# Kernel tuning notes

Measured on AMD Instinct MI355X. Metric: run time of the kernel, lower is better.

Reference implementation:

```python
import jax, jax.numpy as jnp
import numpy as np

PT, SKIP, CNN_UNITS, RNN_UNITS = 16, 32, 512, 512


def setup_inputs() -> dict:
    key = jax.random.key(0)
    k_x, k_w, k_u = jax.random.split(key, 3)
    B, T, C, H = 128, 512, CNN_UNITS, RNN_UNITS
    # 0.05 scaling keeps the relu GRU recurrence numerically stable
    x = jax.random.normal(k_x, (B, T, C), dtype=jnp.float32)
    W = jax.random.normal(k_w, (C, 3 * H), dtype=jnp.float32) * 0.05
    U = jax.random.normal(k_u, (H, 3 * H), dtype=jnp.float32) * 0.05
    b = jnp.zeros((2, 3 * H), dtype=jnp.float32)  # [input_bias, recurrent_bias] (reset_after=True)
    return {"x": x, "W": W, "U": U, "b": b}


def reference(x, W, U, b):
    B, T, C = x.shape
    H = U.shape[0]
    pt, skip = PT, SKIP
    # pretrans: last pt*skip steps -> (B, pt, skip, C) -> (B, skip, pt, C) -> (B*skip, pt, C)
    s = x[:, -pt * skip:, :]
    s = s.reshape(B, pt, skip, C).transpose(0, 2, 1, 3).reshape(B * skip, pt, C)
    # precompute input projections for all timesteps: (pt, B*skip, 3H)
    xp = jnp.einsum('ntc,ch->tnh', s, W) + b[0]
    b_rec = b[1]

    def step(h, xt):
        rec = h @ U + b_rec                      # (N, 3H)
        xz, xr, xh = jnp.split(xt, 3, axis=-1)
        rz, rr, rh = jnp.split(rec, 3, axis=-1)
        z = jax.nn.sigmoid(xz + rz)
        r = jax.nn.sigmoid(xr + rr)
        hh = jax.nn.relu(xh + r * rh)            # activation='relu'
        h_new = z * h + (1.0 - z) * hh
        return h_new, None

    h0 = jnp.zeros((B * skip, H), dtype=x.dtype)
    h_final, _ = jax.lax.scan(step, h0, xp)
    # posttrans: (B*skip, H) -> (B, skip*H)
    return h_final.reshape(B, skip * H)
```

## Files before the change

kernel.cpp:

```cpp
#include <hip/hip_runtime.h>
#include <cstddef>


typedef unsigned short u16;
typedef __attribute__((ext_vector_type(8))) short short8;
typedef __attribute__((ext_vector_type(8))) u16 u16x8;
typedef __attribute__((ext_vector_type(4))) float floatx4;

#define MFMA16(a, b, c) __builtin_amdgcn_mfma_f32_16x16x32_bf16((a), (b), (c), 0, 0, 0)

__device__ __forceinline__ u16 f32_to_bf16(float f) {
  union { float f; unsigned int u; } c; c.f = f;
  unsigned int u = c.u + 0x7FFFu + ((c.u >> 16) & 1u);
  return (u16)(u >> 16);
}
__device__ __forceinline__ float bf16_to_f32(u16 v) {
  union { unsigned int u; float f; } c; c.u = ((unsigned int)v) << 16;
  return c.f;
}
__device__ __forceinline__ float sigmoidf_(float x) {
  return 1.0f / (1.0f + __expf(-x));
}
__device__ __forceinline__ void gload_lds16(const void* g, void* l) {
  __builtin_amdgcn_global_load_lds(
      (const __attribute__((address_space(1))) unsigned int*)g,
      (__attribute__((address_space(3))) unsigned int*)l, 16, 0, 0);
}

__global__ __launch_bounds__(256)
void pack_x(const float* __restrict__ x, u16* __restrict__ xb) {
  __shared__ u16 sm[64 * 512];
  const int t = blockIdx.x >> 6;
  const int nb = blockIdx.x & 63;
  const int tid = threadIdx.x;
#pragma unroll
  for (int it = 0; it < 16; ++it) {
    int idx = it * 256 + tid;
    int row = idx >> 6, ch = idx & 63;
    int xrow = (nb * 2 + (row >> 5)) * 512 + t * 32 + (row & 31);
    const float* src = x + (size_t)xrow * 512 + ch * 8;
    floatx4 va = *(const floatx4*)src;
    floatx4 vb = *(const floatx4*)(src + 4);
    u16x8 pk;
    pk[0] = f32_to_bf16(va[0]); pk[1] = f32_to_bf16(va[1]);
    pk[2] = f32_to_bf16(va[2]); pk[3] = f32_to_bf16(va[3]);
    pk[4] = f32_to_bf16(vb[0]); pk[5] = f32_to_bf16(vb[1]);
    pk[6] = f32_to_bf16(vb[2]); pk[7] = f32_to_bf16(vb[3]);
    *(u16x8*)&sm[row * 512 + (ch ^ (row & 7)) * 8] = pk;
  }
  __syncthreads();
  u16* dst = xb + (size_t)blockIdx.x * 32768;
#pragma unroll
  for (int it = 0; it < 16; ++it) {
    int idx = it * 256 + tid;
    int row = idx & 63, g = (idx >> 6) & 3, kt = idx >> 8;
    int ch = kt * 4 + g;
    u16x8 vv = *(const u16x8*)&sm[row * 512 + (ch ^ (row & 7)) * 8];
    *(u16x8*)(dst + (size_t)idx * 8) = vv;
  }
}

__global__ void pack_Bt(const float* __restrict__ W, const float* __restrict__ U,
                        u16* __restrict__ Bt) {
  size_t gid = (size_t)blockIdx.x * 256 + threadIdx.x;
  int col = (int)(gid & 63);
  int g   = (int)((gid >> 6) & 3);
  int kt  = (int)((gid >> 8) & 31);
  int cc  = (int)(gid >> 13);
  int c = cc * 64 + col;
  int k0 = kt * 32 + g * 8;
  u16x8 pk;
#pragma unroll
  for (int j = 0; j < 8; ++j) {
    int k = k0 + j;
    float v = (k < 512) ? W[(size_t)k * 1536 + c] : U[(size_t)(k - 512) * 1536 + c];
    pk[j] = f32_to_bf16(v);
  }
  *(u16x8*)(Bt + gid * 8) = pk;
}

__global__ __launch_bounds__(256)
void gru_step(const u16* __restrict__ xb, const u16* __restrict__ Bt,
              const float* __restrict__ bias,
              const u16* __restrict__ h_in, u16* __restrict__ h_out,
              float* __restrict__ out, int t, int first, int last) {
  __shared__ alignas(16) char sm[32768];
  const int tid = threadIdx.x;
  const int idx = blockIdx.x;
  const int nb = ((idx >> 6) << 3) | (idx & 7);
  const int hb = (idx >> 3) & 7;
  const int w = __builtin_amdgcn_readfirstlane(tid >> 6);
  const int lane = tid & 63;
  const int wy = w >> 1, wx = w & 1;
  const int q = lane >> 4, lc = lane & 15;

  const u16* xbB = xb + (size_t)(t * 64 + nb) * 32768;
  const u16* htB = h_in + (size_t)nb * 32768;
  const int cs0 = hb, cs1 = 8 + hb, cs2 = 16 + hb;

  floatx4 acZ[2][2] = {{{0.f,0.f,0.f,0.f},{0.f,0.f,0.f,0.f}},{{0.f,0.f,0.f,0.f},{0.f,0.f,0.f,0.f}}};
  floatx4 acR[2][2] = {{{0.f,0.f,0.f,0.f},{0.f,0.f,0.f,0.f}},{{0.f,0.f,0.f,0.f},{0.f,0.f,0.f,0.f}}};
  floatx4 acX[2][2] = {{{0.f,0.f,0.f,0.f},{0.f,0.f,0.f,0.f}},{{0.f,0.f,0.f,0.f},{0.f,0.f,0.f,0.f}}};
  floatx4 acH[2][2] = {{{0.f,0.f,0.f,0.f},{0.f,0.f,0.f,0.f}},{{0.f,0.f,0.f,0.f},{0.f,0.f,0.f,0.f}}};

  const int ktall = first ? 16 : 32;
  const int wo = w * 1024;

  auto stage = [&](int kt, int bsel) {
    char* lds = sm + bsel * 16384;
    const char* aS = (const char*)((kt < 16) ? (xbB + (size_t)kt * 2048)
                                             : (htB + (size_t)(kt - 16) * 2048));
    gload_lds16(aS + wo + lane * 16, lds + wo);
    gload_lds16((const char*)(Bt + (size_t)(cs0 * 32 + kt) * 2048) + wo + lane * 16,
                lds + 4096 + wo);
    gload_lds16((const char*)(Bt + (size_t)(cs1 * 32 + kt) * 2048) + wo + lane * 16,
                lds + 8192 + wo);
    gload_lds16((const char*)(Bt + (size_t)(cs2 * 32 + kt) * 2048) + wo + lane * 16,
                lds + 12288 + wo);
  };

  auto compute = [&](int bsel, floatx4 (&acT)[2][2]) {
    const char* lds = sm + bsel * 16384;
    short8 a0 = *(const short8*)(lds + (q * 64 + wy * 32 + lc) * 16);
    short8 a1 = *(const short8*)(lds + (q * 64 + wy * 32 + 16 + lc) * 16);
#pragma unroll
    for (int ci = 0; ci < 2; ++ci) {
      int co = (q * 64 + wx * 32 + ci * 16 + lc) * 16;
      short8 bz = *(const short8*)(lds + 4096 + co);
      short8 br = *(const short8*)(lds + 8192 + co);
      short8 bh = *(const short8*)(lds + 12288 + co);
      acZ[0][ci] = MFMA16(a0, bz, acZ[0][ci]);
      acZ[1][ci] = MFMA16(a1, bz, acZ[1][ci]);
      acR[0][ci] = MFMA16(a0, br, acR[0][ci]);
      acR[1][ci] = MFMA16(a1, br, acR[1][ci]);
      acT[0][ci] = MFMA16(a0, bh, acT[0][ci]);
      acT[1][ci] = MFMA16(a1, bh, acT[1][ci]);
    }
  };

  stage(0, 0);
  __syncthreads();
  for (int kt = 0; kt < 16; ++kt) {
    if (kt + 1 < ktall) stage(kt + 1, (kt + 1) & 1);
    compute(kt & 1, acX);
    __syncthreads();
  }
  if (!first) {
    for (int kt = 16; kt < 32; ++kt) {
      if (kt + 1 < 32) stage(kt + 1, (kt + 1) & 1);
      compute(kt & 1, acH);
      __syncthreads();
    }
  }

  const float* b0 = bias;
  const float* b1 = bias + 1536;
  u16* Ct = (u16*)sm;
#pragma unroll
  for (int ci = 0; ci < 2; ++ci) {
    const int hcl = wx * 32 + ci * 16 + lc;
    const int hg = hb * 64 + hcl;
    const float bz = b0[hg] + b1[hg];
    const float br = b0[512 + hg] + b1[512 + hg];
    const float b0h = b0[1024 + hg];
    const float b1h = b1[1024 + hg];
    const int ktg = hg >> 5;
    const int gg = (hg >> 3) & 3;
    const size_t hbase = (((size_t)nb * 16 + ktg) * 4 + gg) * 64;
#pragma unroll
    for (int mi = 0; mi < 2; ++mi) {
#pragma unroll
      for (int reg = 0; reg < 4; ++reg) {
        const int nl = wy * 32 + mi * 16 + q * 4 + reg;
        const int n = nb * 64 + nl;
        float z = sigmoidf_(acZ[mi][ci][reg] + bz);
        float r = sigmoidf_(acR[mi][ci][reg] + br);
        float hh = acX[mi][ci][reg] + b0h + r * (acH[mi][ci][reg] + b1h);
        hh = fmaxf(hh, 0.0f);
        float hp = 0.0f;
        if (!first) hp = bf16_to_f32(h_in[(hbase + nl) * 8 + (hg & 7)]);
        float v = z * hp + (1.0f - z) * hh;
        if (last) out[(size_t)n * 512 + hg] = v;
        else      Ct[nl * 72 + hcl] = f32_to_bf16(v);
      }
    }
  }
  if (!last) {
    __syncthreads();
#pragma unroll
    for (int i = 0; i < 2; ++i) {
      int e = i * 256 + tid;
      int row = e & 63;
      int g = (e >> 6) & 3;
      int ktl = e >> 8;
      u16x8 vv = *(const u16x8*)(Ct + row * 72 + ktl * 32 + g * 8);
      *(u16x8*)(h_out + ((((size_t)nb * 16 + (hb * 2 + ktl)) * 4 + g) * 64 + row) * 8) = vv;
    }
  }
}

extern "C" void kernel_launch(void* const* d_in, const int* in_sizes, int n_in,
                              void* d_out, int out_size, void* d_ws, size_t ws_size,
                              hipStream_t stream) {
  const float* x = (const float*)d_in[0];
  const float* W = (const float*)d_in[1];
  const float* U = (const float*)d_in[2];
  const float* bias = (const float*)d_in[3];
  float* out = (float*)d_out;

  u16* xb = (u16*)d_ws;
  u16* Bt = xb + (size_t)16 * 64 * 32768;
  u16* h0 = Bt + (size_t)1536 * 1024;
  u16* h1 = h0 + (size_t)4096 * 512;

  pack_x<<<1024, 256, 0, stream>>>(x, xb);
  pack_Bt<<<768, 256, 0, stream>>>(W, U, Bt);

  for (int t = 0; t < 16; ++t) {
    const u16* hin = (t & 1) ? h1 : h0;
    u16* hout = (t & 1) ? h0 : h1;
    gru_step<<<512, 256, 0, stream>>>(
        xb, Bt, bias, hin, hout, out, t, (t == 0) ? 1 : 0, (t == 15) ? 1 : 0);
  }
}
```

Measured before the change: 523.6 us.

## Load MFMA operands directly from global into registers, dropping LDS staging

Replaces the double-buffered global-to-LDS staging with per-wave direct global loads of A and B fragments into registers, prefetching the next k-chunk while issuing MFMAs. This removes the per-iteration __syncthreads and the LDS round trip, and shrinks shared memory to the output transpose buffer, which may raise occupancy. The cost is that each operand is now fetched by two waves instead of being shared through LDS, so the block issues more global/L2 traffic, and there is less latency hiding than with LDS double buffering.

After: 611.9 us. 16.9% more time.

```diff
diff --git a/kernel.cpp b/kernel.cpp
--- a/kernel.cpp
+++ b/kernel.cpp
@@ -20,11 +20,6 @@
 }
 __device__ __forceinline__ float sigmoidf_(float x) {
   return 1.0f / (1.0f + __expf(-x));
-}
-__device__ __forceinline__ void gload_lds16(const void* g, void* l) {
-  __builtin_amdgcn_global_load_lds(
-      (const __attribute__((address_space(1))) unsigned int*)g,
-      (__attribute__((address_space(3))) unsigned int*)l, 16, 0, 0);
 }
 
 __global__ __launch_bounds__(256)
@@ -84,78 +79,68 @@
               const float* __restrict__ bias,
               const u16* __restrict__ h_in, u16* __restrict__ h_out,
               float* __restrict__ out, int t, int first, int last) {
-  __shared__ alignas(16) char sm[32768];
+  __shared__ alignas(16) u16 Ct[64 * 72];
   const int tid = threadIdx.x;
   const int idx = blockIdx.x;
   const int nb = ((idx >> 6) << 3) | (idx & 7);
   const int hb = (idx >> 3) & 7;
-  const int w = __builtin_amdgcn_readfirstlane(tid >> 6);
   const int lane = tid & 63;
-  const int wy = w >> 1, wx = w & 1;
+  const int wy = (tid >> 7) & 1, wx = (tid >> 6) & 1;
   const int q = lane >> 4, lc = lane & 15;
 
-  const u16* xbB = xb + (size_t)(t * 64 + nb) * 32768;
-  const u16* htB = h_in + (size_t)nb * 32768;
-  const int cs0 = hb, cs1 = 8 + hb, cs2 = 16 + hb;
+  const int aoff = (q * 64 + wy * 32 + lc) * 8;
+  const int boff = (q * 64 + wx * 32 + lc) * 8;
+
+  const u16* pAx = xb + (size_t)(t * 64 + nb) * 32768 + aoff;
+  const u16* pAh = h_in + (size_t)nb * 32768 + aoff;
+  const u16* pBz = Bt + (size_t)(hb +  0) * 65536 + boff;
+  const u16* pBr = Bt + (size_t)(hb +  8) * 65536 + boff;
+  const u16* pBh = Bt + (size_t)(hb + 16) * 65536 + boff;
 
   floatx4 acZ[2][2] = {{{0.f,0.f,0.f,0.f},{0.f,0.f,0.f,0.f}},{{0.f,0.f,0.f,0.f},{0.f,0.f,0.f,0.f}}};
   floatx4 acR[2][2] = {{{0.f,0.f,0.f,0.f},{0.f,0.f,0.f,0.f}},{{0.f,0.f,0.f,0.f},{0.f,0.f,0.f,0.f}}};
   floatx4 acX[2][2] = {{{0.f,0.f,0.f,0.f},{0.f,0.f,0.f,0.f}},{{0.f,0.f,0.f,0.f},{0.f,0.f,0.f,0.f}}};
   floatx4 acH[2][2] = {{{0.f,0.f,0.f,0.f},{0.f,0.f,0.f,0.f}},{{0.f,0.f,0.f,0.f},{0.f,0.f,0.f,0.f}}};
 
-  const int ktall = first ? 16 : 32;
-  const int wo = w * 1024;
-
-  auto stage = [&](int kt, int bsel) {
-    char* lds = sm + bsel * 16384;
-    const char* aS = (const char*)((kt < 16) ? (xbB + (size_t)kt * 2048)
-                                             : (htB + (size_t)(kt - 16) * 2048));
-    gload_lds16(aS + wo + lane * 16, lds + wo);
-    gload_lds16((const char*)(Bt + (size_t)(cs0 * 32 + kt) * 2048) + wo + lane * 16,
-                lds + 4096 + wo);
-    gload_lds16((const char*)(Bt + (size_t)(cs1 * 32 + kt) * 2048) + wo + lane * 16,
-                lds + 8192 + wo);
-    gload_lds16((const char*)(Bt + (size_t)(cs2 * 32 + kt) * 2048) + wo + lane * 16,
-                lds + 12288 + wo);
+  const int nch = first ? 16 : 32;
+
+  short8 a0, a1, bz0, bz1, br0, br1, bh0, bh1;
+  auto loadf = [&](int kt) {
+    const u16* pa = (kt < 16) ? (pAx + (size_t)kt * 2048)
+                              : (pAh + (size_t)(kt - 16) * 2048);
+    const size_t bo = (size_t)kt * 2048;
+    a0  = *(const short8*)(pa);
+    a1  = *(const short8*)(pa + 128);
+    bz0 = *(const short8*)(pBz + bo);
+    bz1 = *(const short8*)(pBz + bo + 128);
+    br0 = *(const short8*)(pBr + bo);
+    br1 = *(const short8*)(pBr + bo + 128);
+    bh0 = *(const short8*)(pBh + bo);
+    bh1 = *(const short8*)(pBh + bo + 128);
   };
 
-  auto compute = [&](int bsel, floatx4 (&acT)[2][2]) {
-    const char* lds = sm + bsel * 16384;
-    short8 a0 = *(const short8*)(lds + (q * 64 + wy * 32 + lc) * 16);
-    short8 a1 = *(const short8*)(lds + (q * 64 + wy * 32 + 16 + lc) * 16);
-#pragma unroll
-    for (int ci = 0; ci < 2; ++ci) {
-      int co = (q * 64 + wx * 32 + ci * 16 + lc) * 16;
-      short8 bz = *(const short8*)(lds + 4096 + co);
-      short8 br = *(const short8*)(lds + 8192 + co);
-      short8 bh = *(const short8*)(lds + 12288 + co);
-      acZ[0][ci] = MFMA16(a0, bz, acZ[0][ci]);
-      acZ[1][ci] = MFMA16(a1, bz, acZ[1][ci]);
-      acR[0][ci] = MFMA16(a0, br, acR[0][ci]);
-      acR[1][ci] = MFMA16(a1, br, acR[1][ci]);
-      acT[0][ci] = MFMA16(a0, bh, acT[0][ci]);
-      acT[1][ci] = MFMA16(a1, bh, acT[1][ci]);
-    }
-  };
-
-  stage(0, 0);
-  __syncthreads();
-  for (int kt = 0; kt < 16; ++kt) {
-    if (kt + 1 < ktall) stage(kt + 1, (kt + 1) & 1);
-    compute(kt & 1, acX);
-    __syncthreads();
-  }
-  if (!first) {
-    for (int kt = 16; kt < 32; ++kt) {
-      if (kt + 1 < 32) stage(kt + 1, (kt + 1) & 1);
-      compute(kt & 1, acH);
-      __syncthreads();
-    }
+  loadf(0);
+  for (int kt = 0; kt < nch; ++kt) {
+    short8 ca0 = a0, ca1 = a1, cz0 = bz0, cz1 = bz1;
+    short8 cr0 = br0, cr1 = br1, ch0 = bh0, ch1 = bh1;
+    if (kt + 1 < nch) loadf(kt + 1);
+    floatx4 (&acT)[2][2] = (kt < 16) ? acX : acH;
+    acZ[0][0] = MFMA16(ca0, cz0, acZ[0][0]);
+    acZ[1][0] = MFMA16(ca1, cz0, acZ[1][0]);
+    acZ[0][1] = MFMA16(ca0, cz1, acZ[0][1]);
+    acZ[1][1] = MFMA16(ca1, cz1, acZ[1][1]);
+    acR[0][0] = MFMA16(ca0, cr0, acR[0][0]);
+    acR[1][0] = MFMA16(ca1, cr0, acR[1][0]);
+    acR[0][1] = MFMA16(ca0, cr1, acR[0][1]);
+    acR[1][1] = MFMA16(ca1, cr1, acR[1][1]);
+    acT[0][0] = MFMA16(ca0, ch0, acT[0][0]);
+    acT[1][0] = MFMA16(ca1, ch0, acT[1][0]);
+    acT[0][1] = MFMA16(ca0, ch1, acT[0][1]);
+    acT[1][1] = MFMA16(ca1, ch1, acT[1][1]);
   }
 
   const float* b0 = bias;
   const float* b1 = bias + 1536;
-  u16* Ct = (u16*)sm;
 #pragma unroll
   for (int ci = 0; ci < 2; ++ci) {
     const int hcl = wx * 32 + ci * 16 + lc;
```
